# Kernel tuning notes

Measured on AMD Instinct MI355X. Metric: run time of the kernel, lower is better.

## Reference

```python
import jax, jax.numpy as jnp
import numpy as np

NUM_PROTEINS = 19000
NUM_DRUGS = 4000
NUM_CELL_LINES = 16
BATCH = 4096
NUM_EDGES = 40000
LAYERS = [2048, 1024, 1]
IN_DIM = 2 * (NUM_PROTEINS + NUM_CELL_LINES)  # 38032


def setup_inputs() -> dict:
    key = jax.random.key(0)
    ks = jax.random.split(key, 10)
    inp = {
        "drug_pairs": jax.random.randint(ks[0], (BATCH, 2), 0, NUM_DRUGS, dtype=jnp.int64 if jax.config.jax_enable_x64 else jnp.int32),
        "cell_lines": jax.random.randint(ks[1], (BATCH,), 0, NUM_CELL_LINES),
        "dpi_drug": jax.random.randint(ks[2], (NUM_EDGES,), 0, NUM_DRUGS),
        "dpi_prot": jax.random.randint(ks[3], (NUM_EDGES,), 0, NUM_PROTEINS),
        "W0": jax.random.normal(ks[4], (LAYERS[0], IN_DIM), dtype=jnp.float32) * 0.02,
        "b0": jnp.zeros((LAYERS[0],), dtype=jnp.float32),
        "W1": jax.random.normal(ks[5], (LAYERS[1], LAYERS[0]), dtype=jnp.float32) * 0.02,
        "b1": jnp.zeros((LAYERS[1],), dtype=jnp.float32),
        "W2": jax.random.normal(ks[6], (LAYERS[2], LAYERS[1]), dtype=jnp.float32) * 0.02,
        "b2": jnp.zeros((LAYERS[2],), dtype=jnp.float32),
    }
    return inp


def _mlp(x, W0, b0, W1, b1, W2, b2):
    h = jax.nn.relu(x @ W0.T + b0)
    h = jax.nn.relu(h @ W1.T + b1)
    return h @ W2.T + b2


def reference(drug_pairs, cell_lines, dpi_drug, dpi_prot, W0, b0, W1, b1, W2, b2):
    # Build drug -> protein multi-hot table with a single vectorized scatter
    # (replaces the per-row Python loop: prot[i, targets] = 1)
    table = jnp.zeros((NUM_DRUGS, NUM_PROTEINS), dtype=jnp.float32)
    table = table.at[dpi_drug, dpi_prot].set(1.0)

    prot_1 = table[drug_pairs[:, 0]]  # [B, P]
    prot_2 = table[drug_pairs[:, 1]]  # [B, P]
    one_hot_cl = jax.nn.one_hot(cell_lines, NUM_CELL_LINES, dtype=jnp.float32)  # [B, C]

    bd1 = jnp.concatenate([prot_1, one_hot_cl], axis=1)
    bd2 = jnp.concatenate([prot_2, one_hot_cl], axis=1)
    x1 = jnp.concatenate([bd1, bd2], axis=1)  # [B, 2*(P+C)]
    x2 = jnp.concatenate([bd2, bd1], axis=1)

    out1 = _mlp(x1, W0, b0, W1, b1, W2, b2)
    out2 = _mlp(x2, W0, b0, W1, b1, W2, b2)
    return (out1[:, 0], out2[:, 0])
```

## Files before the change

### kernel.cpp

```cpp
#include <hip/hip_runtime.h>
#include <hip/hip_bf16.h>
#include <stdint.h>

#define NPROT 19000
#define NDRUG 4000
#define NCELL 16
#define BATCH 4096
#define NEDGE 40000
#define L0 2048
#define L1DIM 1024
#define INDIM 38032
#define HALFDIM 19016
#define DCAP 96
#define BMWORDS ((NDRUG * NPROT + 31) / 32)
#define PQ 4752
#define QSLOT 4752
#define QSTRIDE 4760

typedef float f32x4 __attribute__((ext_vector_type(4)));
typedef short s16x8 __attribute__((ext_vector_type(8)));

__global__ void zero_all_kernel(int* __restrict__ p, int n) {
    int i = blockIdx.x * 256 + threadIdx.x;
    if (i < n) p[i] = 0;
}

__global__ void scatter_dedup_kernel(const int* __restrict__ drug, const int* __restrict__ prot,
                                     unsigned* __restrict__ bitmap, int* __restrict__ cnt4,
                                     int* __restrict__ cntTot, unsigned short* __restrict__ dlist) {
    int e = blockIdx.x * 256 + threadIdx.x;
    if (e < NEDGE) {
        int d = drug[e], p = prot[e];
        unsigned idx = (unsigned)d * NPROT + p;
        unsigned bit = 1u << (idx & 31u);
        unsigned old = atomicOr(&bitmap[idx >> 5], bit);
        if (!(old & bit)) {
            int q = p / PQ;
            atomicAdd(&cnt4[d * 4 + q], 1);
            int pos = atomicAdd(&cntTot[d], 1);
            if (pos < DCAP) dlist[d * DCAP + pos] = (unsigned short)p;
        }
    }
}

__global__ __launch_bounds__(512) void stream_meta_kernel(const int* __restrict__ cnt4,
                                                          int* __restrict__ wlen,
                                                          int* __restrict__ wbase,
                                                          int* __restrict__ pref,
                                                          int* __restrict__ tcnt) {
    __shared__ int wl[32];
    int t = threadIdx.x;
    if (t < 32) wl[t] = 0;
    __syncthreads();
    int c0 = 0, c1 = 0, c2 = 0, c3 = 0;
#pragma unroll
    for (int k = 0; k < 8; ++k) {
        int d = t + (k << 9);
        int pb = ((t << 3) + k) * 4;
        pref[pb + 0] = c0;
        pref[pb + 1] = c1;
        pref[pb + 2] = c2;
        pref[pb + 3] = c3;
        if (d < NDRUG) {
            int n0 = cnt4[d * 4 + 0], n1 = cnt4[d * 4 + 1];
            int n2 = cnt4[d * 4 + 2], n3 = cnt4[d * 4 + 3];
            c0 += n0 ? n0 : 1;
            c1 += n1 ? n1 : 1;
            c2 += n2 ? n2 : 1;
            c3 += n3 ? n3 : 1;
        }
    }
    tcnt[t * 4 + 0] = c0;
    tcnt[t * 4 + 1] = c1;
    tcnt[t * 4 + 2] = c2;
    tcnt[t * 4 + 3] = c3;
    atomicMax(&wl[(t >> 6) * 4 + 0], c0);
    atomicMax(&wl[(t >> 6) * 4 + 1], c1);
    atomicMax(&wl[(t >> 6) * 4 + 2], c2);
    atomicMax(&wl[(t >> 6) * 4 + 3], c3);
    __syncthreads();
    if (t == 0) {
        int run = 0;
        for (int s = 0; s < 32; ++s) {
            wlen[s] = wl[s];
            wbase[s] = run;
            run += wl[s] * 64;
        }
    }
}

__global__ __launch_bounds__(256) void fill_stream_kernel(const int* __restrict__ cnt4,
                                                          const unsigned short* __restrict__ dlist,
                                                          const int* __restrict__ wbase,
                                                          const int* __restrict__ wlen,
                                                          const int* __restrict__ pref,
                                                          const int* __restrict__ tcnt,
                                                          unsigned short* __restrict__ estream) {
    int g = blockIdx.x * 256 + threadIdx.x;
    if (g < NDRUG) {
        int d = g;
        int t = d & 511, k = d >> 9;
        int wv = t >> 6, lane = t & 63;
        int n[4], bases[4], idx[4], j[4];
#pragma unroll
        for (int q = 0; q < 4; ++q) {
            n[q] = cnt4[d * 4 + q];
            bases[q] = wbase[wv * 4 + q] + lane;
            idx[q] = pref[((t << 3) + k) * 4 + q];
            j[q] = 0;
        }
        int ntot = min(n[0] + n[1] + n[2] + n[3], DCAP);
        for (int i = 0; i < ntot; ++i) {
            int p = dlist[d * DCAP + i];
            int q = p / PQ;
            int lp = p - q * PQ;
            unsigned short e = (unsigned short)(lp | ((j[q] == n[q] - 1) ? 0x8000 : 0));
            estream[bases[q] + (idx[q] + j[q]) * 64] = e;
            j[q]++;
        }
#pragma unroll
        for (int q = 0; q < 4; ++q)
            if (n[q] == 0) estream[bases[q] + idx[q] * 64] = (unsigned short)(QSLOT | 0x8000);
    } else if (g < NDRUG + 2048) {
        int idx = g - NDRUG;
        int t = idx >> 2, q = idx & 3;
        int wv = t >> 6;
        int base = wbase[wv * 4 + q] + (t & 63);
        int wlq = wlen[wv * 4 + q];
        for (int jj = tcnt[t * 4 + q]; jj < wlq; ++jj)
            estream[base + jj * 64] = (unsigned short)QSLOT;
    }
}

__global__ void base_kernel(const float* __restrict__ W0, const float* __restrict__ b0,
                            float* __restrict__ BASE) {
    int i = blockIdx.x * 256 + threadIdx.x;
    if (i < NCELL * L0) {
        int c = i >> 11, ch = i & 2047;
        const float* wr = W0 + (size_t)ch * INDIM;
        BASE[(size_t)c * L0 + ch] = b0[ch] + wr[NPROT + c] + wr[HALFDIM + NPROT + c];
    }
}

__device__ inline unsigned bfpair(float a, float b) {
    unsigned ua = __float_as_uint(a), ub = __float_as_uint(b);
    ua += 0x7fffu + ((ua >> 16) & 1u);
    ub += 0x7fffu + ((ub >> 16) & 1u);
    return (ua >> 16) | (ub & 0xffff0000u);
}
__device__ inline float bflo(unsigned w) { return __uint_as_float(w << 16); }
__device__ inline float bfhi(unsigned w) { return __uint_as_float(w & 0xffff0000u); }

__global__ __launch_bounds__(512) void drug_sum_kernel(const float* __restrict__ W0,
                                                       const unsigned short* __restrict__ estream,
                                                       const int* __restrict__ wbase,
                                                       const int* __restrict__ wlen,
                                                       uint2* __restrict__ SAT) {
    __shared__ float wst[4 * QSTRIDE];
    int t = threadIdx.x;
    int bid = blockIdx.x;
    int pq = bid >> 10;
    int k3 = bid & 1023;
    int hb = k3 >> 9;
    int quad = k3 & 511;
    int ch0 = quad * 4;
    size_t colbase = (size_t)hb * HALFDIM + (size_t)pq * PQ;

    int wv = t >> 6;
    int sid = wv * 4 + pq;
    int base = wbase[sid] + (t & 63);
    int wl = wlen[sid];
    int nfull = wl >> 3, rem = wl & 7;
    unsigned e[8];
    if (nfull > 0) {
#pragma unroll
        for (int k = 0; k < 8; ++k) e[k] = estream[base + k * 64];
        base += 512;
    }

#pragma unroll
    for (int c = 0; c < 4; ++c) {
        const float* src = W0 + (size_t)(ch0 + c) * INDIM + colbase;
        for (int i = t * 4; i < PQ; i += 2048) {
            __builtin_amdgcn_global_load_lds(
                (const __attribute__((address_space(1))) void*)(src + i),
                (__attribute__((address_space(3))) void*)(&wst[c * QSTRIDE + i]), 16, 0, 0);
        }
    }
    if (t < 32) wst[(t >> 3) * QSTRIDE + QSLOT + (t & 7)] = 0.f;
    __syncthreads();

    float x0 = 0.f, x1 = 0.f, x2 = 0.f, x3 = 0.f;
    int kk = 0;
    uint2* dstT = SAT + (size_t)bid * 4096;

    auto procBatch = [&](const unsigned* ev) {
        float w0[8], w1[8], w2[8], w3[8];
#pragma unroll
        for (int k = 0; k < 8; ++k) {
            int p = ev[k] & 0x7fffu;
            w0[k] = wst[p];
            w1[k] = wst[QSTRIDE + p];
            w2[k] = wst[2 * QSTRIDE + p];
            w3[k] = wst[3 * QSTRIDE + p];
        }
#pragma unroll
        for (int k = 0; k < 8; ++k) {
            x0 += w0[k];
            x1 += w1[k];
            x2 += w2[k];
            x3 += w3[k];
            if (ev[k] & 0x8000u) {
                uint2 v;
                v.x = bfpair(x0, x1);
                v.y = bfpair(x2, x3);
                dstT[t + (kk << 9)] = v;
                ++kk; x0 = 0.f; x1 = 0.f; x2 = 0.f; x3 = 0.f;
            }
        }
    };

    if (nfull > 0) {
        for (int it = 1; it < nfull; ++it) {
            unsigned f[8];
#pragma unroll
            for (int k = 0; k < 8; ++k) f[k] = estream[base + k * 64];
            base += 512;
            procBatch(e);
#pragma unroll
            for (int k = 0; k < 8; ++k) e[k] = f[k];
        }
        procBatch(e);
    }
    for (int k = 0; k < rem; ++k) {
        unsigned ev = estream[base + k * 64];
        int p = ev & 0x7fffu;
        x0 += wst[p];
        x1 += wst[QSTRIDE + p];
        x2 += wst[2 * QSTRIDE + p];
        x3 += wst[3 * QSTRIDE + p];
        if (ev & 0x8000u) {
            uint2 v;
            v.x = bfpair(x0, x1);
            v.y = bfpair(x2, x3);
            dstT[t + (kk << 9)] = v;
            ++kk; x0 = 0.f; x1 = 0.f; x2 = 0.f; x3 = 0.f;
        }
    }
}

__global__ __launch_bounds__(256) void combine_kernel(const uint2* __restrict__ SAT,
                                                      __hip_bfloat16* __restrict__ SAb,
                                                      __hip_bfloat16* __restrict__ SBb) {
    __shared__ float tile[4][32][33];
    int b = blockIdx.x;
    int hb = b / 2000;
    int rem = b % 2000;
    int q0 = (rem / 125) * 32;
    int d0 = (rem % 125) * 32;
    int tx = threadIdx.x & 31, ty = threadIdx.x >> 5;
#pragma unroll
    for (int r = 0; r < 32; r += 8) {
        int quad = q0 + r + ty;
        float s0 = 0.f, s1 = 0.f, s2 = 0.f, s3 = 0.f;
#pragma unroll
        for (int pq = 0; pq < 4; ++pq) {
            uint2 a = SAT[(size_t)(pq * 1024 + hb * 512 + quad) * 4096 + d0 + tx];
            s0 += bflo(a.x);
            s1 += bfhi(a.x);
            s2 += bflo(a.y);
            s3 += bfhi(a.y);
        }
        tile[0][r + ty][tx] = s0;
        tile[1][r + ty][tx] = s1;
        tile[2][r + ty][tx] = s2;
        tile[3][r + ty][tx] = s3;
    }
    __syncthreads();
    __hip_bfloat16* out = hb ? SBb : SAb;
#pragma unroll
    for (int r = 0; r < 32; r += 8) {
        int d = d0 + r + ty;
        float x = tile[0][tx][r + ty];
        float y = tile[1][tx][r + ty];
        float z = tile[2][tx][r + ty];
        float w = tile[3][tx][r + ty];
        uint2 v;
        v.x = bfpair(x, y);
        v.y = bfpair(z, w);
        *(uint2*)(out + (size_t)d * L0 + (q0 + tx) * 4) = v;
    }
}

__global__ void cvtw1_kernel(const float* __restrict__ W1, __hip_bfloat16* __restrict__ W1b) {
    int i = blockIdx.x * 256 + threadIdx.x;
    const int n = L1DIM * L0 / 4;
    if (i < n) {
        float4 v = ((const float4*)W1)[i];
        uint2 q;
        q.x = bfpair(v.x, v.y);
        q.y = bfpair(v.z, v.w);
        ((uint2*)W1b)[i] = q;
    }
}

__global__ __launch_bounds__(256) void build_h_kernel(const int* __restrict__ dp,
                                                      const int* __restrict__ cl,
                                                      const __hip_bfloat16* __restrict__ SAb,
                                                      const __hip_bfloat16* __restrict__ SBb,
                                                      const float* __restrict__ BASE,
                                                      __hip_bfloat16* __restrict__ h1) {
    int b = blockIdx.x;
    int d1 = dp[2 * b], d2 = dp[2 * b + 1], c = cl[b];
    int ch = threadIdx.x * 8;
    const float* bs = BASE + (size_t)c * L0 + ch;
    uint4 ua1 = *(const uint4*)(SAb + (size_t)d1 * L0 + ch);
    uint4 ua2 = *(const uint4*)(SAb + (size_t)d2 * L0 + ch);
    uint4 us1 = *(const uint4*)(SBb + (size_t)d1 * L0 + ch);
    uint4 us2 = *(const uint4*)(SBb + (size_t)d2 * L0 + ch);
    float4 vb0 = *(const float4*)(bs);
    float4 vb1 = *(const float4*)(bs + 4);
    float bsv[8] = {vb0.x, vb0.y, vb0.z, vb0.w, vb1.x, vb1.y, vb1.z, vb1.w};
    unsigned a1w[4] = {ua1.x, ua1.y, ua1.z, ua1.w};
    unsigned a2w[4] = {ua2.x, ua2.y, ua2.z, ua2.w};
    unsigned s1w[4] = {us1.x, us1.y, us1.z, us1.w};
    unsigned s2w[4] = {us2.x, us2.y, us2.z, us2.w};
    float z1[8], z2[8];
#pragma unroll
    for (int k = 0; k < 4; ++k) {
        z1[2 * k]     = fmaxf(bsv[2 * k]     + bflo(a1w[k]) + bflo(s2w[k]), 0.f);
        z1[2 * k + 1] = fmaxf(bsv[2 * k + 1] + bfhi(a1w[k]) + bfhi(s2w[k]), 0.f);
        z2[2 * k]     = fmaxf(bsv[2 * k]     + bflo(a2w[k]) + bflo(s1w[k]), 0.f);
        z2[2 * k + 1] = fmaxf(bsv[2 * k + 1] + bfhi(a2w[k]) + bfhi(s1w[k]), 0.f);
    }
    uint4 o1, o2;
    o1.x = bfpair(z1[0], z1[1]); o1.y = bfpair(z1[2], z1[3]);
    o1.z = bfpair(z1[4], z1[5]); o1.w = bfpair(z1[6], z1[7]);
    o2.x = bfpair(z2[0], z2[1]); o2.y = bfpair(z2[2], z2[3]);
    o2.z = bfpair(z2[4], z2[5]); o2.w = bfpair(z2[6], z2[7]);
    *(uint4*)((__hip_bfloat16*)h1 + (size_t)b * L0 + ch) = o1;
    *(uint4*)((__hip_bfloat16*)h1 + (size_t)(BATCH + b) * L0 + ch) = o2;
}

__global__ void init_out_kernel(float* __restrict__ out, const float* __restrict__ b2, int n) {
    int i = blockIdx.x * 256 + threadIdx.x;
    if (i < n) out[i] = b2[0];
}

#define BM 128
#define BN 128
#define BK2 64
__global__ __launch_bounds__(256) void gemm_kernel(const __hip_bfloat16* __restrict__ A,
                                                   const __hip_bfloat16* __restrict__ B,
                                                   const float* __restrict__ bias,
                                                   const float* __restrict__ W2,
                                                   float* __restrict__ out,
                                                   int M, int N, int K) {
    __shared__ __hip_bfloat16 As[BM * BK2];
    __shared__ __hip_bfloat16 Bs[BN * BK2];
    int t = threadIdx.x;
    int bid = blockIdx.x;
    int xcd = bid & 7, ii2 = bid >> 3;
    int by = xcd * 8 + (ii2 >> 3);
    int bx = ii2 & 7;
    int brow = by * BM, bcol = bx * BN;
    int w = t >> 6, l = t & 63;
    int wr = w >> 1, wc = w & 1;
    f32x4 acc[4][4] = {};
    int row = l & 15, ko = (l >> 4) * 8;
    int swz = (row & 7) * 8;
    for (int k0 = 0; k0 < K; k0 += BK2) {
#pragma unroll
        for (int i = 0; i < 4; ++i) {
            int idx = i * 256 + t;
            int r = idx >> 3;
            int cb = ((idx & 7) ^ (r & 7)) * 8;
            __builtin_amdgcn_global_load_lds(
                (const __attribute__((address_space(1))) void*)(A + (size_t)(brow + r) * K + k0 + cb),
                (__attribute__((address_space(3))) void*)(&As[idx * 8]), 16, 0, 0);
            __builtin_amdgcn_global_load_lds(
                (const __attribute__((address_space(1))) void*)(B + (size_t)(bcol + r) * K + k0 + cb),
                (__attribute__((address_space(3))) void*)(&Bs[idx * 8]), 16, 0, 0);
        }
        __syncthreads();
#pragma unroll
        for (int ks = 0; ks < 2; ++ks) {
            int col = (ks * 32 + ko) ^ swz;
            s16x8 af[4], bfr[4];
#pragma unroll
            for (int m = 0; m < 4; ++m)
                af[m] = *(const s16x8*)(&As[(wr * 64 + m * 16 + row) * BK2 + col]);
#pragma unroll
            for (int n = 0; n < 4; ++n)
                bfr[n] = *(const s16x8*)(&Bs[(wc * 64 + n * 16 + row) * BK2 + col]);
#pragma unroll
            for (int m = 0; m < 4; ++m)
#pragma unroll
                for (int n = 0; n < 4; ++n)
                    acc[m][n] = __builtin_amdgcn_mfma_f32_16x16x32_bf16(af[m], bfr[n], acc[m][n], 0, 0, 0);
        }
        __syncthreads();
    }
    int cr = (l >> 4) * 4;
    int cc = l & 15;
#pragma unroll
    for (int m = 0; m < 4; ++m) {
        float s[4] = {0.f, 0.f, 0.f, 0.f};
#pragma unroll
        for (int n = 0; n < 4; ++n) {
            int gcol = bcol + wc * 64 + n * 16 + cc;
            float bv = bias[gcol];
            float wv = W2[gcol];
#pragma unroll
            for (int j = 0; j < 4; ++j) {
                float v = fmaxf(acc[m][n][j] + bv, 0.f);
                s[j] += v * wv;
            }
        }
#pragma unroll
        for (int mask = 1; mask < 16; mask <<= 1) {
#pragma unroll
            for (int j = 0; j < 4; ++j) s[j] += __shfl_xor(s[j], mask);
        }
        if (cc == 0) {
            int grow = brow + wr * 64 + m * 16 + cr;
#pragma unroll
            for (int j = 0; j < 4; ++j) atomicAdd(&out[grow + j], s[j]);
        }
    }
}

extern "C" void kernel_launch(void* const* d_in, const int* in_sizes, int n_in,
                              void* d_out, int out_size, void* d_ws, size_t ws_size,
                              hipStream_t stream) {
    const int* drug_pairs = (const int*)d_in[0];
    const int* cell_lines = (const int*)d_in[1];
    const int* dpi_drug = (const int*)d_in[2];
    const int* dpi_prot = (const int*)d_in[3];
    const float* W0 = (const float*)d_in[4];
    const float* b0 = (const float*)d_in[5];
    const float* W1 = (const float*)d_in[6];
    const float* b1 = (const float*)d_in[7];
    const float* W2 = (const float*)d_in[8];
    const float* b2 = (const float*)d_in[9];
    float* out = (float*)d_out;

    char* ws = (char*)d_ws;
    size_t off = 0;
    auto alloc = [&](size_t bytes) {
        char* p = ws + off;
        off += (bytes + 255) & ~(size_t)255;
        return p;
    };
    __hip_bfloat16* SAb = (__hip_bfloat16*)alloc((size_t)NDRUG * L0 * 2);
    __hip_bfloat16* SBb = (__hip_bfloat16*)alloc((size_t)NDRUG * L0 * 2);
    uint2* SAT = (uint2*)alloc((size_t)4096 * 4096 * 8);
    float* BASE = (float*)alloc((size_t)NCELL * L0 * 4);
    __hip_bfloat16* W1b = (__hip_bfloat16*)alloc((size_t)L1DIM * L0 * 2);
    __hip_bfloat16* h1 = (__hip_bfloat16*)alloc((size_t)2 * BATCH * L0 * 2);
    const int ZREG_N = BMWORDS + 5 * NDRUG;
    int* zreg = (int*)alloc((size_t)ZREG_N * 4);
    unsigned* bitmap = (unsigned*)zreg;
    int* cnt4 = zreg + BMWORDS;
    int* cntTot = zreg + BMWORDS + 4 * NDRUG;
    unsigned short* dlist = (unsigned short*)alloc((size_t)NDRUG * DCAP * 2);
    int* wlen = (int*)alloc(32 * 4);
    int* wbase = (int*)alloc(32 * 4);
    int* pref = (int*)alloc((size_t)512 * 8 * 4 * 4);
    int* tcnt = (int*)alloc((size_t)512 * 4 * 4);
    unsigned short* estream = (unsigned short*)alloc((size_t)64 * (NEDGE + 4 * NDRUG + 4096) * 2);

    zero_all_kernel<<<(ZREG_N + 255) / 256, 256, 0, stream>>>(zreg, ZREG_N);
    scatter_dedup_kernel<<<(NEDGE + 255) / 256, 256, 0, stream>>>(dpi_drug, dpi_prot,
                                                                  bitmap, cnt4, cntTot, dlist);
    stream_meta_kernel<<<1, 512, 0, stream>>>(cnt4, wlen, wbase, pref, tcnt);
    fill_stream_kernel<<<(NDRUG + 2048 + 255) / 256, 256, 0, stream>>>(cnt4, dlist, wbase,
                                                                       wlen, pref, tcnt, estream);
    base_kernel<<<(NCELL * L0 + 255) / 256, 256, 0, stream>>>(W0, b0, BASE);
    drug_sum_kernel<<<4096, 512, 0, stream>>>(W0, estream, wbase, wlen, SAT);
    combine_kernel<<<4000, 256, 0, stream>>>(SAT, SAb, SBb);
    cvtw1_kernel<<<(L1DIM * L0 / 4 + 255) / 256, 256, 0, stream>>>(W1, W1b);
    build_h_kernel<<<BATCH, 256, 0, stream>>>(drug_pairs, cell_lines, SAb, SBb, BASE, h1);
    init_out_kernel<<<(2 * BATCH + 255) / 256, 256, 0, stream>>>(out, b2, 2 * BATCH);
    gemm_kernel<<<(2 * BATCH / BM) * (L1DIM / BN), 256, 0, stream>>>(h1, W1b, b1, W2, out,
                                                                     2 * BATCH, L1DIM, L0);
}
```

Before: 242.6 us.

## Process eight channels per block with bf16-packed LDS weights in drug_sum

drug_sum now handles eight W0 channels per block instead of four. It stages them into LDS as bf16 pairs packed into a uint4 per protein column, so each edge costs one 16-byte LDS read instead of four scalar reads, and the grid is halved. The combine kernel is adapted to the uint4 partial-sum layout. This cuts the number of edge-stream passes and LDS transactions. In exchange, the W0 load becomes a synchronous register round-trip instead of a direct global-to-LDS copy, and the weights are rounded to bf16 before accumulation.

```diff
diff --git a/kernel.cpp b/kernel.cpp
--- a/kernel.cpp
+++ b/kernel.cpp
@@ -15,7 +15,7 @@
 #define BMWORDS ((NDRUG * NPROT + 31) / 32)
 #define PQ 4752
 #define QSLOT 4752
-#define QSTRIDE 4760
+#define QN 4760
 
 typedef float f32x4 __attribute__((ext_vector_type(4)));
 typedef short s16x8 __attribute__((ext_vector_type(8)));
@@ -151,144 +151,171 @@
 __device__ inline float bflo(unsigned w) { return __uint_as_float(w << 16); }
 __device__ inline float bfhi(unsigned w) { return __uint_as_float(w & 0xffff0000u); }
 
-__global__ __launch_bounds__(512) void drug_sum_kernel(const float* __restrict__ W0,
-                                                       const unsigned short* __restrict__ estream,
-                                                       const int* __restrict__ wbase,
-                                                       const int* __restrict__ wlen,
-                                                       uint2* __restrict__ SAT) {
-    __shared__ float wst[4 * QSTRIDE];
+__global__ __launch_bounds__(512, 4) void drug_sum_kernel(const float* __restrict__ W0,
+                                                          const unsigned short* __restrict__ estream,
+                                                          const int* __restrict__ wbase,
+                                                          const int* __restrict__ wlen,
+                                                          uint4* __restrict__ SAT) {
+    __shared__ uint4 wst[QN];
     int t = threadIdx.x;
     int bid = blockIdx.x;
-    int pq = bid >> 10;
-    int k3 = bid & 1023;
-    int hb = k3 >> 9;
-    int quad = k3 & 511;
-    int ch0 = quad * 4;
+    int pq = bid >> 9;
+    int k3 = bid & 511;
+    int hb = k3 >> 8;
+    int oct = k3 & 255;
+    int ch0 = oct * 8;
     size_t colbase = (size_t)hb * HALFDIM + (size_t)pq * PQ;
 
     int wv = t >> 6;
     int sid = wv * 4 + pq;
     int base = wbase[sid] + (t & 63);
     int wl = wlen[sid];
-    int nfull = wl >> 3, rem = wl & 7;
-    unsigned e[8];
+    int nfull = wl >> 2, rem = wl & 3;
+    unsigned e[4];
     if (nfull > 0) {
 #pragma unroll
-        for (int k = 0; k < 8; ++k) e[k] = estream[base + k * 64];
-        base += 512;
-    }
-
-#pragma unroll
-    for (int c = 0; c < 4; ++c) {
-        const float* src = W0 + (size_t)(ch0 + c) * INDIM + colbase;
-        for (int i = t * 4; i < PQ; i += 2048) {
-            __builtin_amdgcn_global_load_lds(
-                (const __attribute__((address_space(1))) void*)(src + i),
-                (__attribute__((address_space(3))) void*)(&wst[c * QSTRIDE + i]), 16, 0, 0);
-        }
-    }
-    if (t < 32) wst[(t >> 3) * QSTRIDE + QSLOT + (t & 7)] = 0.f;
+        for (int k = 0; k < 4; ++k) e[k] = estream[base + k * 64];
+        base += 256;
+    }
+
+    const float* s0 = W0 + (size_t)(ch0 + 0) * INDIM + colbase;
+    const float* s1 = W0 + (size_t)(ch0 + 1) * INDIM + colbase;
+    const float* s2 = W0 + (size_t)(ch0 + 2) * INDIM + colbase;
+    const float* s3 = W0 + (size_t)(ch0 + 3) * INDIM + colbase;
+    const float* s4 = W0 + (size_t)(ch0 + 4) * INDIM + colbase;
+    const float* s5 = W0 + (size_t)(ch0 + 5) * INDIM + colbase;
+    const float* s6 = W0 + (size_t)(ch0 + 6) * INDIM + colbase;
+    const float* s7 = W0 + (size_t)(ch0 + 7) * INDIM + colbase;
+    auto stage4 = [&](int i) {
+        float4 a0 = *(const float4*)(s0 + i);
+        float4 a1 = *(const float4*)(s1 + i);
+        float4 a2 = *(const float4*)(s2 + i);
+        float4 a3 = *(const float4*)(s3 + i);
+        float4 a4 = *(const float4*)(s4 + i);
+        float4 a5 = *(const float4*)(s5 + i);
+        float4 a6 = *(const float4*)(s6 + i);
+        float4 a7 = *(const float4*)(s7 + i);
+        const float* f0 = (const float*)&a0;
+        const float* f1 = (const float*)&a1;
+        const float* f2 = (const float*)&a2;
+        const float* f3 = (const float*)&a3;
+        const float* f4 = (const float*)&a4;
+        const float* f5 = (const float*)&a5;
+        const float* f6 = (const float*)&a6;
+        const float* f7 = (const float*)&a7;
+#pragma unroll
+        for (int j = 0; j < 4; ++j) {
+            uint4 q;
+            q.x = bfpair(f0[j], f1[j]);
+            q.y = bfpair(f2[j], f3[j]);
+            q.z = bfpair(f4[j], f5[j]);
+            q.w = bfpair(f6[j], f7[j]);
+            wst[i + j] = q;
+        }
+    };
+    stage4(t * 4);
+    stage4(t * 4 + 2048);
+    {
+        int i = t * 4 + 4096;
+        if (i < PQ) stage4(i);
+    }
+    if (t < 8) { uint4 z; z.x = 0; z.y = 0; z.z = 0; z.w = 0; wst[QSLOT + t] = z; }
     __syncthreads();
 
     float x0 = 0.f, x1 = 0.f, x2 = 0.f, x3 = 0.f;
+    float x4 = 0.f, x5 = 0.f, x6 = 0.f, x7 = 0.f;
     int kk = 0;
-    uint2* dstT = SAT + (size_t)bid * 4096;
-
+    uint4* dstT = SAT + (size_t)bid * 4096;
+
+    auto flush = [&]() {
+        uint4 v;
+        v.x = bfpair(x0, x1);
+        v.y = bfpair(x2, x3);
+        v.z = bfpair(x4, x5);
+        v.w = bfpair(x6, x7);
+        dstT[t + (kk << 9)] = v;
+        ++kk;
+        x0 = x1 = x2 = x3 = x4 = x5 = x6 = x7 = 0.f;
+    };
+    auto acc = [&](uint4 w) {
+        x0 += bflo(w.x); x1 += bfhi(w.x);
+        x2 += bflo(w.y); x3 += bfhi(w.y);
+        x4 += bflo(w.z); x5 += bfhi(w.z);
+        x6 += bflo(w.w); x7 += bfhi(w.w);
+    };
     auto procBatch = [&](const unsigned* ev) {
-        float w0[8], w1[8], w2[8], w3[8];
-#pragma unroll
-        for (int k = 0; k < 8; ++k) {
-            int p = ev[k] & 0x7fffu;
-            w0[k] = wst[p];
-            w1[k] = wst[QSTRIDE + p];
-            w2[k] = wst[2 * QSTRIDE + p];
-            w3[k] = wst[3 * QSTRIDE + p];
-        }
-#pragma unroll
-        for (int k = 0; k < 8; ++k) {
-            x0 += w0[k];
-            x1 += w1[k];
-            x2 += w2[k];
-            x3 += w3[k];
-            if (ev[k] & 0x8000u) {
-                uint2 v;
-                v.x = bfpair(x0, x1);
-                v.y = bfpair(x2, x3);
-                dstT[t + (kk << 9)] = v;
-                ++kk; x0 = 0.f; x1 = 0.f; x2 = 0.f; x3 = 0.f;
-            }
+        uint4 w[4];
+#pragma unroll
+        for (int k = 0; k < 4; ++k) w[k] = wst[ev[k] & 0x7fffu];
+#pragma unroll
+        for (int k = 0; k < 4; ++k) {
+            acc(w[k]);
+            if (ev[k] & 0x8000u) flush();
         }
     };
 
     if (nfull > 0) {
         for (int it = 1; it < nfull; ++it) {
-            unsigned f[8];
-#pragma unroll
-            for (int k = 0; k < 8; ++k) f[k] = estream[base + k * 64];
-            base += 512;
+            unsigned f[4];
+#pragma unroll
+            for (int k = 0; k < 4; ++k) f[k] = estream[base + k * 64];
+            base += 256;
             procBatch(e);
 #pragma unroll
-            for (int k = 0; k < 8; ++k) e[k] = f[k];
+            for (int k = 0; k < 4; ++k) e[k] = f[k];
         }
         procBatch(e);
     }
     for (int k = 0; k < rem; ++k) {
         unsigned ev = estream[base + k * 64];
-        int p = ev & 0x7fffu;
-        x0 += wst[p];
-        x1 += wst[QSTRIDE + p];
-        x2 += wst[2 * QSTRIDE + p];
-        x3 += wst[3 * QSTRIDE + p];
-        if (ev & 0x8000u) {
-            uint2 v;
-            v.x = bfpair(x0, x1);
-            v.y = bfpair(x2, x3);
-            dstT[t + (kk << 9)] = v;
-            ++kk; x0 = 0.f; x1 = 0.f; x2 = 0.f; x3 = 0.f;
-        }
-    }
-}
-
-__global__ __launch_bounds__(256) void combine_kernel(const uint2* __restrict__ SAT,
+        acc(wst[ev & 0x7fffu]);
+        if (ev & 0x8000u) flush();
+    }
+}
+
+__global__ __launch_bounds__(256) void combine_kernel(const uint4* __restrict__ SAT,
                                                       __hip_bfloat16* __restrict__ SAb,
                                                       __hip_bfloat16* __restrict__ SBb) {
-    __shared__ float tile[4][32][33];
+    __shared__ float tile[8][32][33];
     int b = blockIdx.x;
-    int hb = b / 2000;
-    int rem = b % 2000;
-    int q0 = (rem / 125) * 32;
+    int hb = b / 1000;
+    int rem = b % 1000;
+    int o0 = (rem / 125) * 32;
     int d0 = (rem % 125) * 32;
     int tx = threadIdx.x & 31, ty = threadIdx.x >> 5;
 #pragma unroll
     for (int r = 0; r < 32; r += 8) {
-        int quad = q0 + r + ty;
+        int oc = o0 + r + ty;
         float s0 = 0.f, s1 = 0.f, s2 = 0.f, s3 = 0.f;
+        float s4 = 0.f, s5 = 0.f, s6 = 0.f, s7 = 0.f;
 #pragma unroll
         for (int pq = 0; pq < 4; ++pq) {
-            uint2 a = SAT[(size_t)(pq * 1024 + hb * 512 + quad) * 4096 + d0 + tx];
-            s0 += bflo(a.x);
-            s1 += bfhi(a.x);
-            s2 += bflo(a.y);
-            s3 += bfhi(a.y);
+            uint4 a = SAT[(size_t)(pq * 512 + hb * 256 + oc) * 4096 + d0 + tx];
+            s0 += bflo(a.x); s1 += bfhi(a.x);
+            s2 += bflo(a.y); s3 += bfhi(a.y);
+            s4 += bflo(a.z); s5 += bfhi(a.z);
+            s6 += bflo(a.w); s7 += bfhi(a.w);
         }
         tile[0][r + ty][tx] = s0;
         tile[1][r + ty][tx] = s1;
         tile[2][r + ty][tx] = s2;
         tile[3][r + ty][tx] = s3;
+        tile[4][r + ty][tx] = s4;
+        tile[5][r + ty][tx] = s5;
+        tile[6][r + ty][tx] = s6;
+        tile[7][r + ty][tx] = s7;
     }
     __syncthreads();
     __hip_bfloat16* out = hb ? SBb : SAb;
 #pragma unroll
     for (int r = 0; r < 32; r += 8) {
         int d = d0 + r + ty;
-        float x = tile[0][tx][r + ty];
-        float y = tile[1][tx][r + ty];
-        float z = tile[2][tx][r + ty];
-        float w = tile[3][tx][r + ty];
-        uint2 v;
-        v.x = bfpair(x, y);
-        v.y = bfpair(z, w);
-        *(uint2*)(out + (size_t)d * L0 + (q0 + tx) * 4) = v;
+        uint4 v;
+        v.x = bfpair(tile[0][tx][r + ty], tile[1][tx][r + ty]);
+        v.y = bfpair(tile[2][tx][r + ty], tile[3][tx][r + ty]);
+        v.z = bfpair(tile[4][tx][r + ty], tile[5][tx][r + ty]);
+        v.w = bfpair(tile[6][tx][r + ty], tile[7][tx][r + ty]);
+        *(uint4*)(out + (size_t)d * L0 + (o0 + tx) * 8) = v;
     }
 }
 
@@ -454,7 +481,7 @@
     };
     __hip_bfloat16* SAb = (__hip_bfloat16*)alloc((size_t)NDRUG * L0 * 2);
     __hip_bfloat16* SBb = (__hip_bfloat16*)alloc((size_t)NDRUG * L0 * 2);
-    uint2* SAT = (uint2*)alloc((size_t)4096 * 4096 * 8);
+    uint4* SAT = (uint4*)alloc((size_t)2048 * 4096 * 16);
     float* BASE = (float*)alloc((size_t)NCELL * L0 * 4);
     __hip_bfloat16* W1b = (__hip_bfloat16*)alloc((size_t)L1DIM * L0 * 2);
     __hip_bfloat16* h1 = (__hip_bfloat16*)alloc((size_t)2 * BATCH * L0 * 2);
@@ -477,8 +504,8 @@
     fill_stream_kernel<<<(NDRUG + 2048 + 255) / 256, 256, 0, stream>>>(cnt4, dlist, wbase,
                                                                        wlen, pref, tcnt, estream);
     base_kernel<<<(NCELL * L0 + 255) / 256, 256, 0, stream>>>(W0, b0, BASE);
-    drug_sum_kernel<<<4096, 512, 0, stream>>>(W0, estream, wbase, wlen, SAT);
-    combine_kernel<<<4000, 256, 0, stream>>>(SAT, SAb, SBb);
+    drug_sum_kernel<<<2048, 512, 0, stream>>>(W0, estream, wbase, wlen, SAT);
+    combine_kernel<<<2000, 256, 0, stream>>>(SAT, SAb, SBb);
     cvtw1_kernel<<<(L1DIM * L0 / 4 + 255) / 256, 256, 0, stream>>>(W1, W1b);
     build_h_kernel<<<BATCH, 256, 0, stream>>>(drug_pairs, cell_lines, SAb, SBb, BASE, h1);
     init_out_kernel<<<(2 * BATCH + 255) / 256, 256, 0, stream>>>(out, b2, 2 * BATCH);
```

New measurement: 248.7 us. 1.03x slower.
